# Optimization experiments

Hardware: AMD Instinct MI355X
Metric: run time of the kernel (lower is better)

The kernel has to match this reference:

```python
import jax, jax.numpy as jnp
import numpy as np

C = 64   # in_channels
KS = 3   # kernel_size


def _wconv(p, W1, b1, W2, b2, W3, b3):
    # 1x1 conv stack: 3 -> 64 -> 256 -> C*KS*KS, ReLU between
    h = jax.nn.relu(jnp.einsum('oc,bchw->bohw', W1, p) + b1[None, :, None, None])
    h = jax.nn.relu(jnp.einsum('oc,bchw->bohw', W2, h) + b2[None, :, None, None])
    h = jnp.einsum('oc,bchw->bohw', W3, h) + b3[None, :, None, None]
    return h  # [1, C*KS*KS, ho, wo]


def setup_inputs() -> dict:
    key = jax.random.key(0)
    k = jax.random.split(key, 8)
    bs, hi, wi = 2, 128, 128
    ho, wo = 512, 512
    x = jax.random.normal(k[0], (bs, C, hi, wi), jnp.float32)
    poseMap = jax.random.normal(k[1], (1, 3, ho, wo), jnp.float32)
    interMapY = jax.random.randint(k[2], (ho, wo), 0, hi)
    interMapX = jax.random.randint(k[3], (ho, wo), 0, wi)
    W1 = jax.random.normal(k[4], (64, 3), jnp.float32) * 0.1
    b1 = jnp.zeros((64,), jnp.float32)
    W2 = jax.random.normal(k[5], (256, 64), jnp.float32) * 0.05
    b2 = jnp.zeros((256,), jnp.float32)
    W3 = jax.random.normal(k[6], (C * KS * KS, 256), jnp.float32) * 0.05
    b3 = jnp.zeros((C * KS * KS,), jnp.float32)
    return {'x': x, 'poseMap': poseMap, 'W1': W1, 'b1': b1, 'W2': W2, 'b2': b2,
            'W3': W3, 'b3': b3, 'interMapY': interMapY, 'interMapX': interMapX}


def reference(x, poseMap, W1, b1, W2, b2, W3, b3, interMapY, interMapX):
    bs, c, hi, wi = x.shape
    ho, wo = interMapY.shape
    # kernel prediction branch (poseMap is detached in the original)
    w = _wconv(jax.lax.stop_gradient(poseMap), W1, b1, W2, b2, W3, b3)
    w = w.reshape(C, KS * KS, ho, wo)
    sw = jax.nn.softmax(w, axis=1)  # softmax over the KS*KS taps
    # unfold(x, KS, padding=KS//2) tap k corresponds to xp[:, :, i + k//KS, j + k%KS]
    pad = KS // 2
    xp = jnp.pad(x, ((0, 0), (0, 0), (pad, pad), (pad, pad)))
    out = jnp.zeros((bs, C, ho, wo), x.dtype)
    for k in range(KS * KS):  # fixed small loop over taps; fuses gather+weight+reduce
        dy, dx = k // KS, k % KS
        g = xp[:, :, interMapY + dy, interMapX + dx]  # [bs, C, ho, wo] paired gather
        out = out + g * sw[None, :, k]  # sw[:, k] -> [C, ho, wo]
    return out
```

## Files before the change

### kernel.cpp

```cpp
#include <hip/hip_runtime.h>
#include <math.h>

#define HO 512
#define WO 512
#define HI 128
#define WI 128
#define CC 64
#define BS 2
#define NPX 64
#define NT 256

#define W2P_ELEMS (16 * 2 * 64 * 8)
#define W3P_ELEMS (36 * 8 * 64 * 8)
#define XT_ELEM_OFF (W2P_ELEMS + W3P_ELEMS)
#define XT_FLOATS (130 * 130 * 128)

typedef __attribute__((ext_vector_type(8))) short short8;
typedef __attribute__((ext_vector_type(4))) float float4v;

__device__ __forceinline__ unsigned short f2bf(float f) {
    unsigned u = __builtin_bit_cast(unsigned, f);
    unsigned r = (u + 0x7FFFu + ((u >> 16) & 1u)) >> 16;
    return (unsigned short)r;
}

__global__ void prepack_zw(const float* __restrict__ W2,
                           const float* __restrict__ W3,
                           unsigned short* __restrict__ wsp,
                           float* __restrict__ xt) {
    const int total = W2P_ELEMS + W3P_ELEMS;
    for (int idx = blockIdx.x * blockDim.x + threadIdx.x; idx < total;
         idx += gridDim.x * blockDim.x) {
        float v;
        if (idx < W2P_ELEMS) {
            int j = idx & 7, lane = (idx >> 3) & 63, rest = idx >> 9;
            int ks = rest & 1, nt = rest >> 1;
            int n = nt * 16 + (lane & 15);
            int k = ks * 32 + (lane >> 4) * 8 + j;
            v = W2[n * 64 + k];
        } else {
            int i2 = idx - W2P_ELEMS;
            int j = i2 & 7, lane = (i2 >> 3) & 63, rest = i2 >> 9;
            int ks = rest & 7, nt = rest >> 3;
            int tap = nt >> 2, ct = nt & 3;
            int row = (ct * 16 + (lane & 15)) * 9 + tap;
            int k = ks * 32 + (lane >> 4) * 8 + j;
            v = W3[row * 256 + k];
        }
        wsp[idx] = f2bf(v);
    }
    float4v z = {0.f, 0.f, 0.f, 0.f};
    float4v* xt4 = (float4v*)xt;
    for (int i = blockIdx.x * blockDim.x + threadIdx.x; i < XT_FLOATS / 4;
         i += gridDim.x * blockDim.x)
        xt4[i] = z;
}

__global__ void prepack_x(const float* __restrict__ x, float* __restrict__ xt) {
    const int tid = blockIdx.x * blockDim.x + threadIdx.x;
    const int pos = tid & 16383;
    const int g   = tid >> 14;
    const int h = pos >> 7, w = pos & 127;
    const float* src = x + pos;
    float4v v0, v1;
    #pragma unroll
    for (int j = 0; j < 4; ++j) v0[j] = src[(size_t)(g * 8 + j) * (HI * WI)];
    #pragma unroll
    for (int j = 0; j < 4; ++j) v1[j] = src[(size_t)(g * 8 + 4 + j) * (HI * WI)];
    float* dst = xt + ((h + 1) * 130 + (w + 1)) * 128 + g * 8;
    *(float4v*)dst = v0;
    *(float4v*)(dst + 4) = v1;
}

__global__ __launch_bounds__(NT, 3)
void fused_main(const float* __restrict__ xt, const float* __restrict__ pose,
                const float* __restrict__ W1, const float* __restrict__ b1,
                const float* __restrict__ b2, const float* __restrict__ b3,
                const int* __restrict__ iY, const int* __restrict__ iX,
                const unsigned short* __restrict__ wsp,
                float* __restrict__ out)
{
    __shared__ char smem[33792 + 17408 + 768 + 512];
    unsigned short (*sH2)[264] = (unsigned short (*)[264])&smem[0];
    unsigned short (*sH1)[72]  = (unsigned short (*)[72])&smem[33792];
    float (*sOut)[2][16][68]   = (float (*)[2][16][68])&smem[33792];
    float (*sP)[NPX]           = (float (*)[NPX])&smem[51200];
    int* sIY                   = (int*)&smem[51968];
    int* sIX                   = (int*)&smem[52224];

    const int t = threadIdx.x;
    const int pixBase = blockIdx.x * NPX;
    const int y  = pixBase / WO;
    const int x0 = pixBase % WO;

    if (t < 192) sP[t >> 6][t & 63] = pose[(t >> 6) * (HO * WO) + pixBase + (t & 63)];
    if (t < 64) sIY[t] = iY[pixBase + t];
    else if (t < 128) sIX[t - 64] = iX[pixBase + t - 64];
    __syncthreads();

    {
        const int p  = t & 63;
        const int og = t >> 6;
        const float p0 = sP[0][p], p1 = sP[1][p], p2 = sP[2][p];
        #pragma unroll
        for (int i = 0; i < 16; i += 2) {
            const int o = og * 16 + i;
            float a0 = fmaf(W1[o * 3 + 2], p2, fmaf(W1[o * 3 + 1], p1, fmaf(W1[o * 3 + 0], p0, b1[o])));
            float a1 = fmaf(W1[o * 3 + 5], p2, fmaf(W1[o * 3 + 4], p1, fmaf(W1[o * 3 + 3], p0, b1[o + 1])));
            a0 = fmaxf(a0, 0.f); a1 = fmaxf(a1, 0.f);
            unsigned pack = (unsigned)f2bf(a0) | ((unsigned)f2bf(a1) << 16);
            *(unsigned*)&sH1[p][o] = pack;
        }
    }
    __syncthreads();

    const int wv = t >> 6, l = t & 63, lm = l & 15, lq = l >> 4;
    const int m0 = wv * 16;

    {
        short8 a0 = *(const short8*)&sH1[m0 + lm][0  + lq * 8];
        short8 a1 = *(const short8*)&sH1[m0 + lm][32 + lq * 8];
        const short8* w2f = (const short8*)wsp;
        #pragma unroll 4
        for (int nt = 0; nt < 16; ++nt) {
            float4v acc = {0.f, 0.f, 0.f, 0.f};
            short8 bf0 = w2f[(nt * 2 + 0) * 64 + l];
            short8 bf1 = w2f[(nt * 2 + 1) * 64 + l];
            acc = __builtin_amdgcn_mfma_f32_16x16x32_bf16(a0, bf0, acc, 0, 0, 0);
            acc = __builtin_amdgcn_mfma_f32_16x16x32_bf16(a1, bf1, acc, 0, 0, 0);
            const float bv = b2[nt * 16 + lm];
            #pragma unroll
            for (int r = 0; r < 4; ++r)
                sH2[m0 + lq * 4 + r][nt * 16 + lm] = f2bf(fmaxf(acc[r] + bv, 0.f));
        }
    }
    __syncthreads();

    int pbase[4];
    #pragma unroll
    for (int r = 0; r < 4; ++r) {
        const int p = m0 + lq * 4 + r;
        pbase[r] = ((sIY[p] + 1) * 130 + (sIX[p] + 1)) * 128;
    }
    const int koff[9] = {-131 * 128, -130 * 128, -129 * 128,
                         -1 * 128,   0,          1 * 128,
                         129 * 128,  130 * 128,  131 * 128};
    const short8* w3f = (const short8*)(wsp + W2P_ELEMS);

    for (int ct = 0; ct < 4; ++ct) {
        float4v accs[9];
        #pragma unroll
        for (int tap = 0; tap < 9; ++tap) accs[tap] = (float4v){0.f, 0.f, 0.f, 0.f};

        #pragma unroll 2
        for (int ks = 0; ks < 8; ++ks) {
            short8 a = *(const short8*)&sH2[m0 + lm][ks * 32 + lq * 8];
            #pragma unroll
            for (int tap = 0; tap < 9; ++tap) {
                short8 b = w3f[(((tap << 2) | ct) * 8 + ks) * 64 + l];
                accs[tap] = __builtin_amdgcn_mfma_f32_16x16x32_bf16(a, b, accs[tap], 0, 0, 0);
            }
        }

        const int c = ct * 16 + lm;
        float bv[9];
        #pragma unroll
        for (int tap = 0; tap < 9; ++tap) bv[tap] = b3[c * 9 + tap];

        float ob0[4], ob1[4];
        #pragma unroll
        for (int r = 0; r < 4; ++r) {
            float lg[9];
            #pragma unroll
            for (int tap = 0; tap < 9; ++tap) lg[tap] = accs[tap][r] + bv[tap];
            float mx = lg[0];
            #pragma unroll
            for (int tap = 1; tap < 9; ++tap) mx = fmaxf(mx, lg[tap]);
            const float* xb = xt + pbase[r] + c;
            float s = 0.f, o0 = 0.f, o1 = 0.f;
            #pragma unroll
            for (int tap = 0; tap < 9; ++tap) {
                const float ev = __expf(lg[tap] - mx);
                s += ev;
                o0 = fmaf(ev, xb[koff[tap]], o0);
                o1 = fmaf(ev, xb[koff[tap] + 64], o1);
            }
            const float inv = 1.f / s;
            ob0[r] = o0 * inv;
            ob1[r] = o1 * inv;
        }

        float (*so)[16][68] = sOut[ct & 1];
        *(float4v*)&so[0][lm][m0 + lq * 4] = (float4v){ob0[0], ob0[1], ob0[2], ob0[3]};
        *(float4v*)&so[1][lm][m0 + lq * 4] = (float4v){ob1[0], ob1[1], ob1[2], ob1[3]};
        __syncthreads();

        const int row = t >> 3;
        const int b   = row >> 4, ch = row & 15;
        const int seg = (t & 7) * 8;
        float4v v0 = *(float4v*)&so[b][ch][seg];
        float4v v1 = *(float4v*)&so[b][ch][seg + 4];
        float* op = out + (((size_t)(b * CC + ct * 16 + ch) * HO) + y) * WO + x0 + seg;
        *(float4v*)op = v0;
        *(float4v*)(op + 4) = v1;
    }
}

extern "C" void kernel_launch(void* const* d_in, const int* in_sizes, int n_in,
                              void* d_out, int out_size, void* d_ws, size_t ws_size,
                              hipStream_t stream) {
    const float* x    = (const float*)d_in[0];
    const float* pose = (const float*)d_in[1];
    const float* W1   = (const float*)d_in[2];
    const float* b1   = (const float*)d_in[3];
    const float* W2   = (const float*)d_in[4];
    const float* b2   = (const float*)d_in[5];
    const float* W3   = (const float*)d_in[6];
    const float* b3   = (const float*)d_in[7];
    const int*   iY   = (const int*)d_in[8];
    const int*   iX   = (const int*)d_in[9];
    float* out = (float*)d_out;
    unsigned short* wsp = (unsigned short*)d_ws;
    float* xt = (float*)((char*)d_ws + XT_ELEM_OFF * sizeof(unsigned short));

    prepack_zw<<<2048, NT, 0, stream>>>(W2, W3, wsp, xt);
    prepack_x<<<1024, NT, 0, stream>>>(x, xt);

    const int nblocks = (HO * WO) / NPX;
    fused_main<<<nblocks, NT, 0, stream>>>(
        xt, pose, W1, b1, b2, b3, iY, iX, wsp, out);
}
```

Baseline: 422.9 us.

## Drop LDS output staging, alias sH1 into sH2, raise occupancy to four blocks

The shared-memory output transpose buffer is removed and each lane writes its four contiguous pixels directly to global memory as a float4. sH1 now aliases the start of sH2, protected by an added barrier, so LDS per block shrinks from about 52KB to about 35KB. Launch bounds rise to 4 blocks per CU. The 18 gather loads per row are hoisted ahead of the softmax, and the b3 bias loads are moved before the MFMA loop, to expose memory-level parallelism. The trade-offs are less coalesced 16-byte global stores and tighter register pressure at the higher occupancy target. A raw s_barrier is also added at the top of each channel-tile iteration.

```diff
diff --git a/kernel.cpp b/kernel.cpp
--- a/kernel.cpp
+++ b/kernel.cpp
@@ -72,7 +72,7 @@
     *(float4v*)(dst + 4) = v1;
 }
 
-__global__ __launch_bounds__(NT, 3)
+__global__ __launch_bounds__(NT, 4)
 void fused_main(const float* __restrict__ xt, const float* __restrict__ pose,
                 const float* __restrict__ W1, const float* __restrict__ b1,
                 const float* __restrict__ b2, const float* __restrict__ b3,
@@ -80,13 +80,12 @@
                 const unsigned short* __restrict__ wsp,
                 float* __restrict__ out)
 {
-    __shared__ char smem[33792 + 17408 + 768 + 512];
+    __shared__ char smem[33792 + 768 + 512];
     unsigned short (*sH2)[264] = (unsigned short (*)[264])&smem[0];
-    unsigned short (*sH1)[72]  = (unsigned short (*)[72])&smem[33792];
-    float (*sOut)[2][16][68]   = (float (*)[2][16][68])&smem[33792];
-    float (*sP)[NPX]           = (float (*)[NPX])&smem[51200];
-    int* sIY                   = (int*)&smem[51968];
-    int* sIX                   = (int*)&smem[52224];
+    unsigned short (*sH1)[72]  = (unsigned short (*)[72])&smem[0];
+    float (*sP)[NPX]           = (float (*)[NPX])&smem[33792];
+    int* sIY                   = (int*)&smem[34560];
+    int* sIX                   = (int*)&smem[34816];
 
     const int t = threadIdx.x;
     const int pixBase = blockIdx.x * NPX;
@@ -120,6 +119,7 @@
     {
         short8 a0 = *(const short8*)&sH1[m0 + lm][0  + lq * 8];
         short8 a1 = *(const short8*)&sH1[m0 + lm][32 + lq * 8];
+        __syncthreads();
         const short8* w2f = (const short8*)wsp;
         #pragma unroll 4
         for (int nt = 0; nt < 16; ++nt) {
@@ -148,6 +148,13 @@
     const short8* w3f = (const short8*)(wsp + W2P_ELEMS);
 
     for (int ct = 0; ct < 4; ++ct) {
+        __builtin_amdgcn_s_barrier();
+
+        const int c = ct * 16 + lm;
+        float bv[9];
+        #pragma unroll
+        for (int tap = 0; tap < 9; ++tap) bv[tap] = b3[c * 9 + tap];
+
         float4v accs[9];
         #pragma unroll
         for (int tap = 0; tap < 9; ++tap) accs[tap] = (float4v){0.f, 0.f, 0.f, 0.f};
@@ -162,47 +169,40 @@
             }
         }
 
-        const int c = ct * 16 + lm;
-        float bv[9];
-        #pragma unroll
-        for (int tap = 0; tap < 9; ++tap) bv[tap] = b3[c * 9 + tap];
-
         float ob0[4], ob1[4];
         #pragma unroll
         for (int r = 0; r < 4; ++r) {
+            const float* xb = xt + pbase[r] + c;
+            float g0[9], g1[9];
+            #pragma unroll
+            for (int tap = 0; tap < 9; ++tap) {
+                g0[tap] = xb[koff[tap]];
+                g1[tap] = xb[koff[tap] + 64];
+            }
             float lg[9];
             #pragma unroll
             for (int tap = 0; tap < 9; ++tap) lg[tap] = accs[tap][r] + bv[tap];
             float mx = lg[0];
             #pragma unroll
             for (int tap = 1; tap < 9; ++tap) mx = fmaxf(mx, lg[tap]);
-            const float* xb = xt + pbase[r] + c;
             float s = 0.f, o0 = 0.f, o1 = 0.f;
             #pragma unroll
             for (int tap = 0; tap < 9; ++tap) {
                 const float ev = __expf(lg[tap] - mx);
                 s += ev;
-                o0 = fmaf(ev, xb[koff[tap]], o0);
-                o1 = fmaf(ev, xb[koff[tap] + 64], o1);
+                o0 = fmaf(ev, g0[tap], o0);
+                o1 = fmaf(ev, g1[tap], o1);
             }
             const float inv = 1.f / s;
             ob0[r] = o0 * inv;
             ob1[r] = o1 * inv;
         }
 
-        float (*so)[16][68] = sOut[ct & 1];
-        *(float4v*)&so[0][lm][m0 + lq * 4] = (float4v){ob0[0], ob0[1], ob0[2], ob0[3]};
-        *(float4v*)&so[1][lm][m0 + lq * 4] = (float4v){ob1[0], ob1[1], ob1[2], ob1[3]};
-        __syncthreads();
-
-        const int row = t >> 3;
-        const int b   = row >> 4, ch = row & 15;
-        const int seg = (t & 7) * 8;
-        float4v v0 = *(float4v*)&so[b][ch][seg];
-        float4v v1 = *(float4v*)&so[b][ch][seg + 4];
-        float* op = out + (((size_t)(b * CC + ct * 16 + ch) * HO) + y) * WO + x0 + seg;
-        *(float4v*)op = v0;
-        *(float4v*)(op + 4) = v1;
+        const int px = x0 + m0 + lq * 4;
+        float* op0 = out + ((size_t)c * HO + y) * WO + px;
+        float* op1 = out + ((size_t)(CC + c) * HO + y) * WO + px;
+        *(float4v*)op0 = (float4v){ob0[0], ob0[1], ob0[2], ob0[3]};
+        *(float4v*)op1 = (float4v){ob1[0], ob1[1], ob1[2], ob1[3]};
     }
 }
 
```

Result: slower. 527.1 us (+24.6%).
